# Optimization experiments

Measured on AMD Instinct MI355X. Metric: run time of the kernel, lower is better.

## Reference

```python
import jax, jax.numpy as jnp
import numpy as np

N_NODES = 100000
N_EDGES = 1600000


def setup_inputs() -> dict:
    key = jax.random.key(0)
    k1, k2, k3, k4, k5, k6 = jax.random.split(key, 6)
    x = jax.random.normal(k1, (N_NODES, 1), dtype=jnp.float32)
    edge_index = jax.random.randint(k2, (2, N_EDGES), 0, N_NODES, dtype=jnp.int64)
    # Glorot-style init scale for GCNConv weights
    W1 = jax.random.normal(k3, (1, 35), dtype=jnp.float32) * 0.5
    b1 = jnp.zeros((35,), dtype=jnp.float32)
    W2 = jax.random.normal(k4, (35, 1), dtype=jnp.float32) * 0.2
    b2 = jnp.zeros((1,), dtype=jnp.float32)
    return {"x": x, "edge_index": edge_index, "W1": W1, "b1": b1, "W2": W2, "b2": b2}


def _gcn_norm(edge_index, num_nodes):
    # PyG GCNConv default: add self-loops (weight 1), symmetric normalization
    loop = jnp.arange(num_nodes, dtype=edge_index.dtype)
    src = jnp.concatenate([edge_index[0], loop])
    dst = jnp.concatenate([edge_index[1], loop])
    ones = jnp.ones(src.shape[0], dtype=jnp.float32)
    deg = jax.ops.segment_sum(ones, dst, num_segments=num_nodes)
    dinv = jnp.where(deg > 0, jax.lax.rsqrt(deg), 0.0)
    norm = dinv[src] * dinv[dst]  # [E+N]
    return src, dst, norm


def _gcn_conv(x, src, dst, norm, W, b, num_nodes):
    h = x @ W                                  # [N, out] dense transform first (out dims small)
    msg = h[src] * norm[:, None]               # gather + scale over edges
    out = jax.ops.segment_sum(msg, dst, num_segments=num_nodes)  # scatter-add
    return out + b


def reference(x, edge_index, W1, b1, W2, b2):
    n = x.shape[0]
    src, dst, norm = _gcn_norm(edge_index, n)
    x1 = jax.nn.sigmoid(_gcn_conv(x, src, dst, norm, W1, b1, n))
    # F.dropout(training=self.training): evaluated in inference mode -> identity
    x2 = jax.nn.sigmoid(_gcn_conv(x1, src, dst, norm, W2, b2, n))
    return x2
```

## Files before the change

### kernel.cpp

```cpp
#include <hip/hip_runtime.h>
#include <math.h>


#define NBLK 512
#define TBE  256
#define TBA  1024
#define MAXB 512

__device__ __forceinline__ int chunk_of(int blk) {
    return ((blk & 7) * (NBLK >> 3)) + (blk >> 3);
}

__global__ __launch_bounds__(TBE)
void k_hist(const int* __restrict__ dst, int* __restrict__ bh,
            int e, int ec, int nb) {
    __shared__ int sh[MAXB];
    const int t = threadIdx.x;
    const int chunk = chunk_of(blockIdx.x);
    for (int i = t; i < nb; i += TBE) sh[i] = 0;
    __syncthreads();
    int start = chunk * ec, end = min(e, start + ec);
    int tile = start;
    for (; tile + TBE * 4 <= end; tile += TBE * 4) {
        const int4 d4 = *reinterpret_cast<const int4*>(dst + tile + t * 4);
        atomicAdd(&sh[d4.x >> 8], 1);
        atomicAdd(&sh[d4.y >> 8], 1);
        atomicAdd(&sh[d4.z >> 8], 1);
        atomicAdd(&sh[d4.w >> 8], 1);
    }
    for (int i = tile + t; i < end; i += TBE) atomicAdd(&sh[dst[i] >> 8], 1);
    __syncthreads();
    for (int i = t; i < nb; i += TBE) bh[(size_t)i * NBLK + chunk] = sh[i];
}

__global__ __launch_bounds__(TBE)
void k_colscan(int* __restrict__ bh, int* __restrict__ bucktot, int nb) {
    const int lane = threadIdx.x & 63;
    const int wid = threadIdx.x >> 6;
    const int b = blockIdx.x * 4 + wid;
    if (b >= nb) return;
    int4* row = reinterpret_cast<int4*>(bh + (size_t)b * NBLK + lane * 8);
    int4 v0 = row[0], v1 = row[1];
    int s = v0.x + v0.y + v0.z + v0.w + v1.x + v1.y + v1.z + v1.w;
    int inc = s;
#pragma unroll
    for (int off = 1; off < 64; off <<= 1) {
        int w = __shfl_up(inc, off, 64);
        if (lane >= off) inc += w;
    }
    int run = inc - s;
    int c;
    c = v0.x; v0.x = run; run += c;  c = v0.y; v0.y = run; run += c;
    c = v0.z; v0.z = run; run += c;  c = v0.w; v0.w = run; run += c;
    c = v1.x; v1.x = run; run += c;  c = v1.y; v1.y = run; run += c;
    c = v1.z; v1.z = run; run += c;  c = v1.w; v1.w = run; run += c;
    row[0] = v0; row[1] = v1;
    if (lane == 63) bucktot[b] = inc;
}

__global__ __launch_bounds__(TBE)
void k_bin(const int* __restrict__ src, const int* __restrict__ dst,
           const int* __restrict__ bh, const int* __restrict__ bucktot,
           int* __restrict__ buckbase, int* __restrict__ packed,
           int e, int ec, int nb) {
    __shared__ int sbase[MAXB];
    __shared__ int wtot[4];
    const int t = threadIdx.x;
    const int lane = t & 63, wid = t >> 6;
    const int chunk = chunk_of(blockIdx.x);

    int i0 = 2 * t, i1 = 2 * t + 1;
    int c0 = (i0 < nb) ? bucktot[i0] : 0;
    int c1 = (i1 < nb) ? bucktot[i1] : 0;
    int tsum = c0 + c1;
    int winc = tsum;
#pragma unroll
    for (int off = 1; off < 64; off <<= 1) {
        int w = __shfl_up(winc, off, 64);
        if (lane >= off) winc += w;
    }
    if (lane == 63) wtot[wid] = winc;
    __syncthreads();
    int wbase = 0;
#pragma unroll
    for (int w = 0; w < 4; ++w) wbase += (w < wid) ? wtot[w] : 0;
    int ex = wbase + winc - tsum;
    if (i0 < nb) sbase[i0] = ex;
    if (i1 < nb) sbase[i1] = ex + c0;
    __syncthreads();

    if (blockIdx.x == 0) {
        for (int i = t; i < nb; i += TBE) buckbase[i] = sbase[i];
        if (t == 0) buckbase[nb] = e;
    }
    for (int i = t; i < nb; i += TBE) sbase[i] += bh[(size_t)i * NBLK + chunk];
    __syncthreads();

    int start = chunk * ec, end = min(e, start + ec);
    int tile = start;
    for (; tile + TBE * 4 <= end; tile += TBE * 4) {
        const int4 s4 = *reinterpret_cast<const int4*>(src + tile + t * 4);
        const int4 d4 = *reinterpret_cast<const int4*>(dst + tile + t * 4);
        int p;
        p = atomicAdd(&sbase[d4.x >> 8], 1); packed[p] = (s4.x << 8) | (d4.x & 255);
        p = atomicAdd(&sbase[d4.y >> 8], 1); packed[p] = (s4.y << 8) | (d4.y & 255);
        p = atomicAdd(&sbase[d4.z >> 8], 1); packed[p] = (s4.z << 8) | (d4.z & 255);
        p = atomicAdd(&sbase[d4.w >> 8], 1); packed[p] = (s4.w << 8) | (d4.w & 255);
    }
    for (int i = tile + t; i < end; i += TBE) {
        int d = dst[i], s = src[i];
        int p = atomicAdd(&sbase[d >> 8], 1);
        packed[p] = (s << 8) | (d & 255);
    }
}

#define SEG_WALK(S0, S1, BODY_PK)                                        \
    {                                                                    \
        int head = min((S1), ((S0) + 3) & ~3);                           \
        for (int j = (S0) + t; j < head; j += TBA) {                     \
            int pk = packed[j]; BODY_PK;                                 \
        }                                                                \
        int nvec = ((S1) - head) >> 2;                                   \
        const int4* pv = reinterpret_cast<const int4*>(packed + head);   \
        for (int j = t; j < nvec; j += TBA) {                            \
            int4 q = pv[j];                                              \
            { int pk = q.x; BODY_PK; }                                   \
            { int pk = q.y; BODY_PK; }                                   \
            { int pk = q.z; BODY_PK; }                                   \
            { int pk = q.w; BODY_PK; }                                   \
        }                                                                \
        for (int j = head + 4 * nvec + t; j < (S1); j += TBA) {          \
            int pk = packed[j]; BODY_PK;                                 \
        }                                                                \
    }

__global__ __launch_bounds__(TBA)
void k_deg(const int* __restrict__ packed, const int* __restrict__ buckbase,
           const float* __restrict__ x, float* __restrict__ dinv,
           float* __restrict__ g, int n) {
    __shared__ int cnt[1024];
    const int t = threadIdx.x, b = blockIdx.x;
    cnt[t] = 0;
    __syncthreads();
    const int bank = (t & 3) << 8;
    int s0 = buckbase[b], s1 = buckbase[b + 1];
    SEG_WALK(s0, s1, atomicAdd(&cnt[bank | (pk & 255)], 1))
    __syncthreads();
    if (t < 256) {
        int node = (b << 8) + t;
        if (node < n) {
            int c = cnt[t] + cnt[256 + t] + cnt[512 + t] + cnt[768 + t];
            float di = rsqrtf(1.0f + (float)c);
            dinv[node] = di;
            g[node] = di * x[node];
        }
    }
}

__global__ __launch_bounds__(TBA)
void k_l1(const int* __restrict__ packed, const int* __restrict__ buckbase,
          const float* __restrict__ g, const float* __restrict__ dinv,
          const float* __restrict__ W1, const float* __restrict__ b1,
          const float* __restrict__ W2, float* __restrict__ u, int n, int K) {
    __shared__ float acc[1024];
    const int t = threadIdx.x, b = blockIdx.x;
    acc[t] = 0.f;
    __syncthreads();
    const int bank = (t & 3) << 8;
    int s0 = buckbase[b], s1 = buckbase[b + 1];
    SEG_WALK(s0, s1, atomicAdd(&acc[bank | (pk & 255)], g[pk >> 8]))
    __syncthreads();
    if (t < 256) {
        int node = (b << 8) + t;
        if (node < n) {
            float s = acc[t] + acc[256 + t] + acc[512 + t] + acc[768 + t];
            float di = dinv[node];
            float tt = di * (s + g[node]);
            float h2 = 0.f;
            for (int k = 0; k < K; ++k) {
                float z = fmaf(W1[k], tt, b1[k]);
                h2 = fmaf(__fdividef(1.f, 1.f + __expf(-z)), W2[k], h2);
            }
            u[node] = di * h2;
        }
    }
}

__global__ __launch_bounds__(TBA)
void k_l2(const int* __restrict__ packed, const int* __restrict__ buckbase,
          const float* __restrict__ u, const float* __restrict__ dinv,
          const float* __restrict__ b2, float* __restrict__ out, int n) {
    __shared__ float acc[1024];
    const int t = threadIdx.x, b = blockIdx.x;
    acc[t] = 0.f;
    __syncthreads();
    const int bank = (t & 3) << 8;
    int s0 = buckbase[b], s1 = buckbase[b + 1];
    SEG_WALK(s0, s1, atomicAdd(&acc[bank | (pk & 255)], u[pk >> 8]))
    __syncthreads();
    if (t < 256) {
        int node = (b << 8) + t;
        if (node < n) {
            float s = acc[t] + acc[256 + t] + acc[512 + t] + acc[768 + t];
            float z = fmaf(dinv[node], s + u[node], b2[0]);
            out[node] = __fdividef(1.f, 1.f + __expf(-z));
        }
    }
}

__global__ void f_init(float* __restrict__ deg, int n) {
    int i = blockIdx.x * 256 + threadIdx.x;
    if (i < n) deg[i] = 1.0f;
}
__global__ void f_degree(const int* __restrict__ dst, float* __restrict__ deg, int e) {
    int i = blockIdx.x * 256 + threadIdx.x;
    if (i < e) atomicAdd(&deg[dst[i]], 1.0f);
}
__global__ void f_node1(const float* __restrict__ x, float* dd,
                        float* __restrict__ g, float* __restrict__ s, int n) {
    int i = blockIdx.x * 256 + threadIdx.x;
    if (i < n) {
        float di = rsqrtf(dd[i]);
        dd[i] = di;
        float gi = di * x[i];
        g[i] = gi; s[i] = gi;
    }
}
__global__ void f_scatter(const int* __restrict__ src, const int* __restrict__ dst,
                          const float* __restrict__ g, float* __restrict__ s, int e) {
    int i = blockIdx.x * 256 + threadIdx.x;
    if (i < e) atomicAdd(&s[dst[i]], g[src[i]]);
}
__global__ void f_node2(const float* __restrict__ dinv, const float* s,
                        const float* __restrict__ W1, const float* __restrict__ b1,
                        const float* __restrict__ W2, float* u, float* r, int n, int K) {
    int i = blockIdx.x * 256 + threadIdx.x;
    if (i < n) {
        float tt = dinv[i] * s[i];
        float h2 = 0.f;
        for (int k = 0; k < K; ++k) {
            float z = fmaf(W1[k], tt, b1[k]);
            h2 = fmaf(__fdividef(1.f, 1.f + __expf(-z)), W2[k], h2);
        }
        float ui = dinv[i] * h2;
        u[i] = ui; r[i] = ui;
    }
}
__global__ void f_out(const float* __restrict__ dinv, const float* __restrict__ r,
                      const float* __restrict__ b2, float* __restrict__ out, int n) {
    int i = blockIdx.x * 256 + threadIdx.x;
    if (i < n) {
        float z = fmaf(dinv[i], r[i], b2[0]);
        out[i] = __fdividef(1.f, 1.f + __expf(-z));
    }
}

extern "C" void kernel_launch(void* const* d_in, const int* in_sizes, int n_in,
                              void* d_out, int out_size, void* d_ws, size_t ws_size,
                              hipStream_t stream) {
    const float* x  = (const float*)d_in[0];
    const int*   ei = (const int*)d_in[1];
    const float* W1 = (const float*)d_in[2];
    const float* b1 = (const float*)d_in[3];
    const float* W2 = (const float*)d_in[4];
    const float* b2 = (const float*)d_in[5];

    const int n = in_sizes[0];
    const int e = in_sizes[1] / 2;
    const int K = in_sizes[2];
    const int* src = ei;
    const int* dst = ei + e;
    float* out = (float*)d_out;

    const int nb = (n + 255) >> 8;
    const int ec = (((e + NBLK - 1) / NBLK) + 3) & ~3;

    size_t need = ((size_t)nb * NBLK + 2 * (size_t)nb + 1 + (size_t)e + 3 * (size_t)n) * 4;

    if (nb <= MAXB && n < (1 << 23) && (e & 3) == 0 && ws_size >= need) {
        int* bh       = (int*)d_ws;
        int* bucktot  = bh + (size_t)nb * NBLK;
        int* buckbase = bucktot + nb;
        int* packed   = buckbase + nb + 1;
        float* dinv   = (float*)(packed + e);
        float* g      = dinv + n;
        float* u      = g + n;

        k_hist   <<<NBLK, TBE, 0, stream>>>(dst, bh, e, ec, nb);
        k_colscan<<<(nb + 3) / 4, TBE, 0, stream>>>(bh, bucktot, nb);
        k_bin    <<<NBLK, TBE, 0, stream>>>(src, dst, bh, bucktot, buckbase,
                                            packed, e, ec, nb);
        k_deg    <<<nb, TBA, 0, stream>>>(packed, buckbase, x, dinv, g, n);
        k_l1     <<<nb, TBA, 0, stream>>>(packed, buckbase, g, dinv, W1, b1, W2, u, n, K);
        k_l2     <<<nb, TBA, 0, stream>>>(packed, buckbase, u, dinv, b2, out, n);
    } else {
        float* A = (float*)d_ws;
        float* B = A + n;
        float* C = B + n;
        const int bn = (n + 255) / 256;
        const int be = (e + 255) / 256;
        f_init   <<<bn, 256, 0, stream>>>(A, n);
        f_degree <<<be, 256, 0, stream>>>(dst, A, e);
        f_node1  <<<bn, 256, 0, stream>>>(x, A, B, C, n);
        f_scatter<<<be, 256, 0, stream>>>(src, dst, B, C, e);
        f_node2  <<<bn, 256, 0, stream>>>(A, C, W1, b1, W2, B, C, n, K);
        f_scatter<<<be, 256, 0, stream>>>(src, dst, B, C, e);
        f_out    <<<bn, 256, 0, stream>>>(A, C, b2, out, n);
    }
}
```

Baseline: 58.05 us.

## Replace global bucket sort with per-chunk local binning and chunk-list aggregation

```diff
diff --git a/kernel.cpp b/kernel.cpp
--- a/kernel.cpp
+++ b/kernel.cpp
@@ -6,78 +6,47 @@
 #define TBE  256
 #define TBA  1024
 #define MAXB 512
-
-__device__ __forceinline__ int chunk_of(int blk) {
-    return ((blk & 7) * (NBLK >> 3)) + (blk >> 3);
-}
-
-__global__ __launch_bounds__(TBE)
-void k_hist(const int* __restrict__ dst, int* __restrict__ bh,
-            int e, int ec, int nb) {
-    __shared__ int sh[MAXB];
-    const int t = threadIdx.x;
-    const int chunk = chunk_of(blockIdx.x);
-    for (int i = t; i < nb; i += TBE) sh[i] = 0;
-    __syncthreads();
-    int start = chunk * ec, end = min(e, start + ec);
-    int tile = start;
-    for (; tile + TBE * 4 <= end; tile += TBE * 4) {
-        const int4 d4 = *reinterpret_cast<const int4*>(dst + tile + t * 4);
-        atomicAdd(&sh[d4.x >> 8], 1);
-        atomicAdd(&sh[d4.y >> 8], 1);
-        atomicAdd(&sh[d4.z >> 8], 1);
-        atomicAdd(&sh[d4.w >> 8], 1);
-    }
-    for (int i = tile + t; i < end; i += TBE) atomicAdd(&sh[dst[i] >> 8], 1);
-    __syncthreads();
-    for (int i = t; i < nb; i += TBE) bh[(size_t)i * NBLK + chunk] = sh[i];
-}
-
-__global__ __launch_bounds__(TBE)
-void k_colscan(int* __restrict__ bh, int* __restrict__ bucktot, int nb) {
-    const int lane = threadIdx.x & 63;
-    const int wid = threadIdx.x >> 6;
-    const int b = blockIdx.x * 4 + wid;
-    if (b >= nb) return;
-    int4* row = reinterpret_cast<int4*>(bh + (size_t)b * NBLK + lane * 8);
-    int4 v0 = row[0], v1 = row[1];
-    int s = v0.x + v0.y + v0.z + v0.w + v1.x + v1.y + v1.z + v1.w;
-    int inc = s;
-#pragma unroll
-    for (int off = 1; off < 64; off <<= 1) {
-        int w = __shfl_up(inc, off, 64);
-        if (lane >= off) inc += w;
-    }
-    int run = inc - s;
-    int c;
-    c = v0.x; v0.x = run; run += c;  c = v0.y; v0.y = run; run += c;
-    c = v0.z; v0.z = run; run += c;  c = v0.w; v0.w = run; run += c;
-    c = v1.x; v1.x = run; run += c;  c = v1.y; v1.y = run; run += c;
-    c = v1.z; v1.z = run; run += c;  c = v1.w; v1.w = run; run += c;
-    row[0] = v0; row[1] = v1;
-    if (lane == 63) bucktot[b] = inc;
-}
+#define QT   4
 
 __global__ __launch_bounds__(TBE)
 void k_bin(const int* __restrict__ src, const int* __restrict__ dst,
-           const int* __restrict__ bh, const int* __restrict__ bucktot,
-           int* __restrict__ buckbase, int* __restrict__ packed,
+           int* __restrict__ packed, int* __restrict__ cnt, int* __restrict__ off,
            int e, int ec, int nb) {
-    __shared__ int sbase[MAXB];
+    __shared__ int sh[MAXB];
     __shared__ int wtot[4];
     const int t = threadIdx.x;
+    const int chunk = blockIdx.x;
+    const int start = chunk * ec;
+    const int end = min(e, start + ec);
+
+    for (int i = t; i < nb; i += TBE) sh[i] = 0;
+    __syncthreads();
+
+    int4 rs[QT], rd[QT];
+#pragma unroll
+    for (int q = 0; q < QT; ++q) {
+        int idx = start + (q * TBE + t) * 4;
+        if (idx < end) {
+            rs[q] = *reinterpret_cast<const int4*>(src + idx);
+            rd[q] = *reinterpret_cast<const int4*>(dst + idx);
+            atomicAdd(&sh[rd[q].x >> 8], 1);
+            atomicAdd(&sh[rd[q].y >> 8], 1);
+            atomicAdd(&sh[rd[q].z >> 8], 1);
+            atomicAdd(&sh[rd[q].w >> 8], 1);
+        }
+    }
+    __syncthreads();
+
     const int lane = t & 63, wid = t >> 6;
-    const int chunk = chunk_of(blockIdx.x);
-
     int i0 = 2 * t, i1 = 2 * t + 1;
-    int c0 = (i0 < nb) ? bucktot[i0] : 0;
-    int c1 = (i1 < nb) ? bucktot[i1] : 0;
+    int c0 = (i0 < nb) ? sh[i0] : 0;
+    int c1 = (i1 < nb) ? sh[i1] : 0;
     int tsum = c0 + c1;
     int winc = tsum;
 #pragma unroll
-    for (int off = 1; off < 64; off <<= 1) {
-        int w = __shfl_up(winc, off, 64);
-        if (lane >= off) winc += w;
+    for (int o = 1; o < 64; o <<= 1) {
+        int w = __shfl_up(winc, o, 64);
+        if (lane >= o) winc += w;
     }
     if (lane == 63) wtot[wid] = winc;
     __syncthreads();
@@ -85,71 +54,57 @@
 #pragma unroll
     for (int w = 0; w < 4; ++w) wbase += (w < wid) ? wtot[w] : 0;
     int ex = wbase + winc - tsum;
-    if (i0 < nb) sbase[i0] = ex;
-    if (i1 < nb) sbase[i1] = ex + c0;
-    __syncthreads();
-
-    if (blockIdx.x == 0) {
-        for (int i = t; i < nb; i += TBE) buckbase[i] = sbase[i];
-        if (t == 0) buckbase[nb] = e;
-    }
-    for (int i = t; i < nb; i += TBE) sbase[i] += bh[(size_t)i * NBLK + chunk];
-    __syncthreads();
-
-    int start = chunk * ec, end = min(e, start + ec);
-    int tile = start;
-    for (; tile + TBE * 4 <= end; tile += TBE * 4) {
-        const int4 s4 = *reinterpret_cast<const int4*>(src + tile + t * 4);
-        const int4 d4 = *reinterpret_cast<const int4*>(dst + tile + t * 4);
-        int p;
-        p = atomicAdd(&sbase[d4.x >> 8], 1); packed[p] = (s4.x << 8) | (d4.x & 255);
-        p = atomicAdd(&sbase[d4.y >> 8], 1); packed[p] = (s4.y << 8) | (d4.y & 255);
-        p = atomicAdd(&sbase[d4.z >> 8], 1); packed[p] = (s4.z << 8) | (d4.z & 255);
-        p = atomicAdd(&sbase[d4.w >> 8], 1); packed[p] = (s4.w << 8) | (d4.w & 255);
-    }
-    for (int i = tile + t; i < end; i += TBE) {
-        int d = dst[i], s = src[i];
-        int p = atomicAdd(&sbase[d >> 8], 1);
-        packed[p] = (s << 8) | (d & 255);
-    }
-}
-
-#define SEG_WALK(S0, S1, BODY_PK)                                        \
-    {                                                                    \
-        int head = min((S1), ((S0) + 3) & ~3);                           \
-        for (int j = (S0) + t; j < head; j += TBA) {                     \
-            int pk = packed[j]; BODY_PK;                                 \
-        }                                                                \
-        int nvec = ((S1) - head) >> 2;                                   \
-        const int4* pv = reinterpret_cast<const int4*>(packed + head);   \
-        for (int j = t; j < nvec; j += TBA) {                            \
-            int4 q = pv[j];                                              \
-            { int pk = q.x; BODY_PK; }                                   \
-            { int pk = q.y; BODY_PK; }                                   \
-            { int pk = q.z; BODY_PK; }                                   \
-            { int pk = q.w; BODY_PK; }                                   \
-        }                                                                \
-        for (int j = head + 4 * nvec + t; j < (S1); j += TBA) {          \
-            int pk = packed[j]; BODY_PK;                                 \
-        }                                                                \
+
+    if (i0 < nb) { cnt[(size_t)i0 * NBLK + chunk] = c0; off[(size_t)i0 * NBLK + chunk] = ex; }
+    if (i1 < nb) { cnt[(size_t)i1 * NBLK + chunk] = c1; off[(size_t)i1 * NBLK + chunk] = ex + c0; }
+    if (i0 < nb) sh[i0] = ex;
+    if (i1 < nb) sh[i1] = ex + c0;
+    __syncthreads();
+
+#pragma unroll
+    for (int q = 0; q < QT; ++q) {
+        int idx = start + (q * TBE + t) * 4;
+        if (idx < end) {
+            int p;
+            p = atomicAdd(&sh[rd[q].x >> 8], 1); packed[start + p] = (rs[q].x << 8) | (rd[q].x & 255);
+            p = atomicAdd(&sh[rd[q].y >> 8], 1); packed[start + p] = (rs[q].y << 8) | (rd[q].y & 255);
+            p = atomicAdd(&sh[rd[q].z >> 8], 1); packed[start + p] = (rs[q].z << 8) | (rd[q].z & 255);
+            p = atomicAdd(&sh[rd[q].w >> 8], 1); packed[start + p] = (rs[q].w << 8) | (rd[q].w & 255);
+        }
+    }
+}
+
+#define AGG_WALK(BODY_PK)                                                 \
+    {                                                                     \
+        const int lane = t & 63;                                          \
+        const int wave = t >> 6;                                          \
+        for (int c = wave; c < NBLK; c += (TBA / 64)) {                   \
+            int cc = shc[c];                                              \
+            int base = c * ec + sho[c];                                   \
+            for (int r = lane; r < cc; r += 64) {                         \
+                int pk = packed[base + r];                                \
+                BODY_PK;                                                  \
+            }                                                             \
+        }                                                                 \
     }
 
 __global__ __launch_bounds__(TBA)
-void k_deg(const int* __restrict__ packed, const int* __restrict__ buckbase,
-           const float* __restrict__ x, float* __restrict__ dinv,
-           float* __restrict__ g, int n) {
-    __shared__ int cnt[1024];
+void k_deg(const int* __restrict__ packed, const int* __restrict__ cnt,
+           const int* __restrict__ off, const float* __restrict__ x,
+           float* __restrict__ dinv, float* __restrict__ g, int n, int ec) {
+    __shared__ int shc[NBLK], sho[NBLK];
+    __shared__ int hist[1024];
     const int t = threadIdx.x, b = blockIdx.x;
-    cnt[t] = 0;
+    if (t < NBLK) { shc[t] = cnt[(size_t)b * NBLK + t]; sho[t] = off[(size_t)b * NBLK + t]; }
+    hist[t] = 0;
     __syncthreads();
     const int bank = (t & 3) << 8;
-    int s0 = buckbase[b], s1 = buckbase[b + 1];
-    SEG_WALK(s0, s1, atomicAdd(&cnt[bank | (pk & 255)], 1))
+    AGG_WALK(atomicAdd(&hist[bank | (pk & 255)], 1))
     __syncthreads();
     if (t < 256) {
         int node = (b << 8) + t;
         if (node < n) {
-            int c = cnt[t] + cnt[256 + t] + cnt[512 + t] + cnt[768 + t];
+            int c = hist[t] + hist[256 + t] + hist[512 + t] + hist[768 + t];
             float di = rsqrtf(1.0f + (float)c);
             dinv[node] = di;
             g[node] = di * x[node];
@@ -158,17 +113,19 @@
 }
 
 __global__ __launch_bounds__(TBA)
-void k_l1(const int* __restrict__ packed, const int* __restrict__ buckbase,
-          const float* __restrict__ g, const float* __restrict__ dinv,
+void k_l1(const int* __restrict__ packed, const int* __restrict__ cnt,
+          const int* __restrict__ off, const float* __restrict__ g,
+          const float* __restrict__ dinv,
           const float* __restrict__ W1, const float* __restrict__ b1,
-          const float* __restrict__ W2, float* __restrict__ u, int n, int K) {
+          const float* __restrict__ W2, float* __restrict__ u, int n, int ec, int K) {
+    __shared__ int shc[NBLK], sho[NBLK];
     __shared__ float acc[1024];
     const int t = threadIdx.x, b = blockIdx.x;
+    if (t < NBLK) { shc[t] = cnt[(size_t)b * NBLK + t]; sho[t] = off[(size_t)b * NBLK + t]; }
     acc[t] = 0.f;
     __syncthreads();
     const int bank = (t & 3) << 8;
-    int s0 = buckbase[b], s1 = buckbase[b + 1];
-    SEG_WALK(s0, s1, atomicAdd(&acc[bank | (pk & 255)], g[pk >> 8]))
+    AGG_WALK(atomicAdd(&acc[bank | (pk & 255)], g[pk >> 8]))
     __syncthreads();
     if (t < 256) {
         int node = (b << 8) + t;
@@ -187,16 +144,18 @@
 }
 
 __global__ __launch_bounds__(TBA)
-void k_l2(const int* __restrict__ packed, const int* __restrict__ buckbase,
-          const float* __restrict__ u, const float* __restrict__ dinv,
-          const float* __restrict__ b2, float* __restrict__ out, int n) {
+void k_l2(const int* __restrict__ packed, const int* __restrict__ cnt,
+          const int* __restrict__ off, const float* __restrict__ u,
+          const float* __restrict__ dinv, const float* __restrict__ b2,
+          float* __restrict__ out, int n, int ec) {
+    __shared__ int shc[NBLK], sho[NBLK];
     __shared__ float acc[1024];
     const int t = threadIdx.x, b = blockIdx.x;
+    if (t < NBLK) { shc[t] = cnt[(size_t)b * NBLK + t]; sho[t] = off[(size_t)b * NBLK + t]; }
     acc[t] = 0.f;
     __syncthreads();
     const int bank = (t & 3) << 8;
-    int s0 = buckbase[b], s1 = buckbase[b + 1];
-    SEG_WALK(s0, s1, atomicAdd(&acc[bank | (pk & 255)], u[pk >> 8]))
+    AGG_WALK(atomicAdd(&acc[bank | (pk & 255)], u[pk >> 8]))
     __syncthreads();
     if (t < 256) {
         int node = (b << 8) + t;
@@ -275,24 +234,20 @@
     const int nb = (n + 255) >> 8;
     const int ec = (((e + NBLK - 1) / NBLK) + 3) & ~3;
 
-    size_t need = ((size_t)nb * NBLK + 2 * (size_t)nb + 1 + (size_t)e + 3 * (size_t)n) * 4;
-
-    if (nb <= MAXB && n < (1 << 23) && (e & 3) == 0 && ws_size >= need) {
-        int* bh       = (int*)d_ws;
-        int* bucktot  = bh + (size_t)nb * NBLK;
-        int* buckbase = bucktot + nb;
-        int* packed   = buckbase + nb + 1;
-        float* dinv   = (float*)(packed + e);
+    size_t need = ((size_t)NBLK * ec + 2 * (size_t)nb * NBLK + 3 * (size_t)n) * 4;
+
+    if (nb <= MAXB && ec <= TBE * 4 * QT && (e & 3) == 0 && ws_size >= need) {
+        int* packed   = (int*)d_ws;
+        int* cnt      = packed + (size_t)NBLK * ec;
+        int* off      = cnt + (size_t)nb * NBLK;
+        float* dinv   = (float*)(off + (size_t)nb * NBLK);
         float* g      = dinv + n;
         float* u      = g + n;
 
-        k_hist   <<<NBLK, TBE, 0, stream>>>(dst, bh, e, ec, nb);
-        k_colscan<<<(nb + 3) / 4, TBE, 0, stream>>>(bh, bucktot, nb);
-        k_bin    <<<NBLK, TBE, 0, stream>>>(src, dst, bh, bucktot, buckbase,
-                                            packed, e, ec, nb);
-        k_deg    <<<nb, TBA, 0, stream>>>(packed, buckbase, x, dinv, g, n);
-        k_l1     <<<nb, TBA, 0, stream>>>(packed, buckbase, g, dinv, W1, b1, W2, u, n, K);
-        k_l2     <<<nb, TBA, 0, stream>>>(packed, buckbase, u, dinv, b2, out, n);
+        k_bin<<<NBLK, TBE, 0, stream>>>(src, dst, packed, cnt, off, e, ec, nb);
+        k_deg<<<nb, TBA, 0, stream>>>(packed, cnt, off, x, dinv, g, n, ec);
+        k_l1 <<<nb, TBA, 0, stream>>>(packed, cnt, off, g, dinv, W1, b1, W2, u, n, ec, K);
+        k_l2 <<<nb, TBA, 0, stream>>>(packed, cnt, off, u, dinv, b2, out, n, ec);
     } else {
         float* A = (float*)d_ws;
         float* B = A + n;
```

Measured after the change: 96.03 us. 1.65x slower.
